# Optimization experiments

Hardware: AMD Instinct MI355X
Metric: run time of the kernel (lower is better)

Reference implementation:

```python
import jax, jax.numpy as jnp
import numpy as np

B, C, H, W = 16, 64, 128, 128
K = 3
Z = 128


def setup_inputs() -> dict:
    key = jax.random.key(0)
    k1, k2, k3, k4 = jax.random.split(key, 4)
    x = jax.random.normal(k1, (B, C, H, W), dtype=jnp.float32)
    z = jax.random.normal(k2, (B, Z), dtype=jnp.float32)
    # generator: Linear(Z -> C*C*K*K), scaled for stable conv outputs
    gen_w = jax.random.normal(k3, (Z, C * C * K * K), dtype=jnp.float32) * 0.02
    gen_b = jax.random.normal(k4, (C * C * K * K,), dtype=jnp.float32) * 0.02
    return {"x": x, "z": z, "gen_w": gen_w, "gen_b": gen_b}


def _conv_one(xi, wi):
    # xi: [C,H,W], wi: [C_out,C_in,K,K]; 'same' padding conv, no bias
    out = jax.lax.conv_general_dilated(
        xi[None], wi, window_strides=(1, 1), padding="SAME",
        dimension_numbers=("NCHW", "OIHW", "NCHW"))
    return out[0]


def reference(x, z, gen_w, gen_b):
    # per-sample weight generation: [B, C*C*K*K] -> [B, C, C, K, K]
    weight = (z @ gen_w + gen_b).reshape(B, C, C, K, K)
    # batched per-sample convolution (replaces the python loop over batch)
    return jax.vmap(_conv_one)(x, weight)
```

## Files before the change

kernel.cpp:

```cpp
#include <hip/hip_runtime.h>
#include <hip/hip_bf16.h>

typedef __attribute__((ext_vector_type(4))) float f32x4;
typedef __attribute__((ext_vector_type(8))) short short8;

#define B_ 16
#define C_ 64
#define H_ 128
#define W_ 128
#define Z_ 128
#define IDXN (C_*C_*9)
#define NT 18

__device__ __forceinline__ unsigned short f2bf(float f) {
  __hip_bfloat16 h = __float2bfloat16(f);
  return *reinterpret_cast<unsigned short*>(&h);
}

__global__ __launch_bounds__(256) void wgen_k(
    const float* __restrict__ z, const float* __restrict__ gw,
    const float* __restrict__ gb, unsigned short* __restrict__ wfrag) {
  __shared__ __align__(16) float zs[B_*Z_];
  int t = threadIdx.x;
#pragma unroll
  for (int i = 0; i < 8; ++i) zs[i*256 + t] = z[i*256 + t];
  __syncthreads();
  int lane = t & 63, bg = t >> 6;
  int b0 = bg*4;
  int idx0 = blockIdx.x*128 + lane;
  float acc[4][2];
  float bv0 = gb[idx0], bv1 = gb[idx0 + 64];
#pragma unroll
  for (int bi = 0; bi < 4; ++bi) { acc[bi][0] = bv0; acc[bi][1] = bv1; }

  for (int z0 = 0; z0 < Z_; z0 += 4) {
    float ga[4], gbv[4];
#pragma unroll
    for (int zi = 0; zi < 4; ++zi) {
      ga[zi]  = gw[(size_t)(z0+zi)*IDXN + idx0];
      gbv[zi] = gw[(size_t)(z0+zi)*IDXN + idx0 + 64];
    }
#pragma unroll
    for (int bi = 0; bi < 4; ++bi) {
      f32x4 zq = *reinterpret_cast<const f32x4*>(&zs[(b0+bi)*Z_ + z0]);
      acc[bi][0] = fmaf(zq[0], ga[0], fmaf(zq[1], ga[1], fmaf(zq[2], ga[2], fmaf(zq[3], ga[3], acc[bi][0]))));
      acc[bi][1] = fmaf(zq[0], gbv[0], fmaf(zq[1], gbv[1], fmaf(zq[2], gbv[2], fmaf(zq[3], gbv[3], acc[bi][1]))));
    }
  }
#pragma unroll
  for (int ni = 0; ni < 2; ++ni) {
    int idx = idx0 + ni*64;
    int kw = idx % 3, r1 = idx/3;
    int kh = r1 % 3, r2 = r1/3;
    int ci = r2 & 63, co = r2 >> 6;
    int k = (kh*3 + kw)*C_ + ci;
    int ts = k >> 5, kin = k & 31;
    int lm = (co & 15) | ((kin >> 3) << 4);
    int j = kin & 7, m = co >> 4;
    int base = ((ts*4 + m)*64 + lm)*8 + j;
#pragma unroll
    for (int bi = 0; bi < 4; ++bi)
      wfrag[(size_t)(b0+bi)*(NT*4*64*8) + base] = f2bf(acc[bi][ni]);
  }
}

__global__ __launch_bounds__(512, 4) void conv_k(
    const float* __restrict__ x,
    const unsigned short* __restrict__ wfrag,
    float* __restrict__ out) {
  __shared__ __align__(16) unsigned char xs[4*130*128];
  int orig = blockIdx.x;
  int blk = (orig & 7)*128 + (orig >> 3);
  int b = blk >> 6;
  int h0 = (blk & 63)*2;
  int tid = threadIdx.x;
  int v = tid >> 6, lane = tid & 63;

  {
    int r = v >> 1, hf = v & 1;
    int hh = h0 - 1 + r;
    bool hv = (hh >= 0) & (hh < H_);
    unsigned char* ldsrow = xs + r*(130*128);
    if (hv) {
      if (lane < 8) {
        int s = hf ? (1032 + lane) : lane;
        uint4 zv; zv.x = 0; zv.y = 0; zv.z = 0; zv.w = 0;
        *reinterpret_cast<uint4*>(ldsrow + s*16) = zv;
      }
      const float* xrow = x + (((size_t)b*C_)*H_ + hh)*W_;
      int w0 = 2*lane, col0 = w0 + 1, col1 = w0 + 2;
      int g = lane >> 3;
#pragma unroll
      for (int i = 0; i < 4; ++i) {
        int chunk = (hf*4 + i + g) & 7;
        float2 v2[8];
#pragma unroll
        for (int j = 0; j < 8; ++j)
          v2[j] = *reinterpret_cast<const float2*>(xrow + (size_t)(chunk*8 + j)*(H_*W_) + w0);
        uint4 o0, o1;
        unsigned short* s0 = reinterpret_cast<unsigned short*>(&o0);
        unsigned short* s1 = reinterpret_cast<unsigned short*>(&o1);
#pragma unroll
        for (int j = 0; j < 8; ++j) {
          s0[j] = f2bf(v2[j].x);
          s1[j] = f2bf(v2[j].y);
        }
        int a0 = col0*128 + (((chunk ^ col0) & 7) << 4);
        int a1 = col1*128 + (((chunk ^ col1) & 7) << 4);
        *reinterpret_cast<uint4*>(ldsrow + a0) = o0;
        *reinterpret_cast<uint4*>(ldsrow + a1) = o1;
      }
    } else {
      uint4 zv; zv.x = 0; zv.y = 0; zv.z = 0; zv.w = 0;
#pragma unroll
      for (int it = 0; it < 9; ++it) {
        int di = it*64 + lane;
        if (di < 520) *reinterpret_cast<uint4*>(ldsrow + (hf*520 + di)*16) = zv;
      }
    }
  }

  int l15 = lane & 15, lhi = lane >> 4;
  int phr = v >> 2, pw0 = ((v >> 1) & 1)*64;
  int mt0 = (v & 1)*2;
  const unsigned short* wb = wfrag + (size_t)b*(NT*4*64*8);

  short8 wf0 = *reinterpret_cast<const short8*>(wb + (((0*4 + mt0 + 0)*64 + lane)*8));
  short8 wf1 = *reinterpret_cast<const short8*>(wb + (((0*4 + mt0 + 1)*64 + lane)*8));

  __syncthreads();

  f32x4 acc[4][2];
#pragma unroll
  for (int mp = 0; mp < 4; ++mp)
#pragma unroll
    for (int nc = 0; nc < 2; ++nc)
      acc[mp][nc] = (f32x4){0.f, 0.f, 0.f, 0.f};

#pragma unroll
  for (int t = 0; t < NT; ++t) {
    int kk = t >> 1, kh = kk/3, kw = kk%3, half = t & 1;
    short8 nf0, nf1;
    if (t + 1 < NT) {
      nf0 = *reinterpret_cast<const short8*>(wb + ((((t+1)*4 + mt0 + 0)*64 + lane)*8));
      nf1 = *reinterpret_cast<const short8*>(wb + ((((t+1)*4 + mt0 + 1)*64 + lane)*8));
    }
    int chunk = half*4 + lhi;
    short8 xa[4];
#pragma unroll
    for (int mp = 0; mp < 4; ++mp) {
      int col = pw0 + mp*16 + l15 + kw;
      int addr = ((phr + kh)*130 + col)*128 + (((chunk ^ col) & 7) << 4);
      xa[mp] = *reinterpret_cast<const short8*>(&xs[addr]);
    }
#pragma unroll
    for (int mp = 0; mp < 4; ++mp) {
      acc[mp][0] = __builtin_amdgcn_mfma_f32_16x16x32_bf16(xa[mp], wf0, acc[mp][0], 0, 0, 0);
      acc[mp][1] = __builtin_amdgcn_mfma_f32_16x16x32_bf16(xa[mp], wf1, acc[mp][1], 0, 0, 0);
    }
    wf0 = nf0; wf1 = nf1;
  }

  int ph = h0 + phr;
#pragma unroll
  for (int nc = 0; nc < 2; ++nc) {
    int co = (mt0 + nc)*16 + l15;
    float* op = out + (((size_t)b*C_ + co)*H_ + ph)*W_;
#pragma unroll
    for (int mp = 0; mp < 4; ++mp) {
      int pix = pw0 + mp*16 + lhi*4;
      *reinterpret_cast<f32x4*>(op + pix) = acc[mp][nc];
    }
  }
}

__global__ void sentinel_k(float* out, int n) {
  int i = blockIdx.x*256 + threadIdx.x;
  if (i < n) out[i] = 1.0e6f;
}

extern "C" void kernel_launch(void* const* d_in, const int* in_sizes, int n_in,
                              void* d_out, int out_size, void* d_ws, size_t ws_size,
                              hipStream_t stream) {
  const float* x  = (const float*)d_in[0];
  const float* z  = (const float*)d_in[1];
  const float* gw = (const float*)d_in[2];
  const float* gb = (const float*)d_in[3];
  float* out = (float*)d_out;

  size_t wfrag_elems = (size_t)B_*IDXN;
  size_t need = wfrag_elems*sizeof(unsigned short);
  if (ws_size < need) {
    sentinel_k<<<(out_size + 255)/256, 256, 0, stream>>>(out, out_size);
    return;
  }
  unsigned short* wfrag = (unsigned short*)d_ws;

  wgen_k <<<IDXN/128, 256, 0, stream>>>(z, gw, gb, wfrag);
  conv_k <<<B_*(H_/2), 512, 0, stream>>>(x, wfrag, out);
}
```

Baseline: 51.23 us.

## Process 8-row bands per block with ring-buffered LDS rows and prefetch

The conv kernel moves from one 2-row tile per 512-thread block to 1024-thread blocks that each walk an 8-row band in four 2-row steps. Input rows live in a 6-slot ring buffer in LDS, and the next two rows are loaded from global memory while the MFMAs for the current step run. The MFMA inner loop is also software-pipelined so LDS fragments for the next tap are loaded one step ahead. The aim is to cut the redundant halo loads (4 rows loaded per 2 output rows) and to hide global load latency. In exchange the grid shrinks to 256 blocks, there is a syncthreads per step, and each wave now does less MFMA work per LDS fragment.

```diff
diff --git a/kernel.cpp b/kernel.cpp
--- a/kernel.cpp
+++ b/kernel.cpp
@@ -9,6 +9,8 @@
 #define H_ 128
 #define W_ 128
 #define Z_ 128
+#define HW_ (H_*W_)
+#define CHW_ (C_*H_*W_)
 #define IDXN (C_*C_*9)
 #define NT 18
 
@@ -64,113 +66,145 @@
   }
 }
 
-__global__ __launch_bounds__(512, 4) void conv_k(
+__global__ __launch_bounds__(1024, 4) void conv_k(
     const float* __restrict__ x,
     const unsigned short* __restrict__ wfrag,
     float* __restrict__ out) {
-  __shared__ __align__(16) unsigned char xs[4*130*128];
+  __shared__ __align__(16) unsigned char xs[6*130*128];
   int orig = blockIdx.x;
-  int blk = (orig & 7)*128 + (orig >> 3);
-  int b = blk >> 6;
-  int h0 = (blk & 63)*2;
+  int blk = (orig & 7)*32 + (orig >> 3);
+  int b = blk >> 4;
+  int band = blk & 15;
+  int hbase = band*8;
   int tid = threadIdx.x;
   int v = tid >> 6, lane = tid & 63;
 
-  {
-    int r = v >> 1, hf = v & 1;
-    int hh = h0 - 1 + r;
-    bool hv = (hh >= 0) & (hh < H_);
-    unsigned char* ldsrow = xs + r*(130*128);
-    if (hv) {
-      if (lane < 8) {
-        int s = hf ? (1032 + lane) : lane;
-        uint4 zv; zv.x = 0; zv.y = 0; zv.z = 0; zv.w = 0;
-        *reinterpret_cast<uint4*>(ldsrow + s*16) = zv;
-      }
-      const float* xrow = x + (((size_t)b*C_)*H_ + hh)*W_;
-      int w0 = 2*lane, col0 = w0 + 1, col1 = w0 + 2;
-      int g = lane >> 3;
-#pragma unroll
-      for (int i = 0; i < 4; ++i) {
-        int chunk = (hf*4 + i + g) & 7;
-        float2 v2[8];
-#pragma unroll
-        for (int j = 0; j < 8; ++j)
-          v2[j] = *reinterpret_cast<const float2*>(xrow + (size_t)(chunk*8 + j)*(H_*W_) + w0);
-        uint4 o0, o1;
-        unsigned short* s0 = reinterpret_cast<unsigned short*>(&o0);
-        unsigned short* s1 = reinterpret_cast<unsigned short*>(&o1);
-#pragma unroll
-        for (int j = 0; j < 8; ++j) {
-          s0[j] = f2bf(v2[j].x);
-          s1[j] = f2bf(v2[j].y);
+  int ri = tid >> 9;
+  int wp = lane;
+  int cig = v & 7;
+  const float* xb = x + (size_t)b*CHW_;
+  int s_base0 = hbase % 6;
+
+  if (tid < 96) {
+    int sl = tid >> 4, cc = (tid >> 3) & 1, ch = tid & 7;
+    int col = cc ? 129 : 0;
+    uint4 zv; zv.x = 0; zv.y = 0; zv.z = 0; zv.w = 0;
+    *reinterpret_cast<uint4*>(&xs[(sl*130 + col)*128 + ch*16]) = zv;
+  }
+
+#pragma unroll
+  for (int s = 0; s < 2; ++s) {
+    int g = hbase - 1 + 2*s + ri;
+    int slw = s_base0 + 2*s + ri; if (slw >= 6) slw -= 6;
+    uint4 o0, o1;
+    o0.x=0;o0.y=0;o0.z=0;o0.w=0; o1=o0;
+    if (g >= 0 && g < H_) {
+      const float* xr = xb + (size_t)g*W_ + 2*wp;
+      unsigned short* p0 = reinterpret_cast<unsigned short*>(&o0);
+      unsigned short* p1 = reinterpret_cast<unsigned short*>(&o1);
+#pragma unroll
+      for (int j = 0; j < 8; ++j) {
+        float2 f = *reinterpret_cast<const float2*>(xr + (size_t)(cig*8 + j)*HW_);
+        p0[j] = f2bf(f.x); p1[j] = f2bf(f.y);
+      }
+    }
+    int c0 = 2*wp + 1, c1 = c0 + 1;
+    *reinterpret_cast<uint4*>(&xs[(slw*130 + c0)*128 + (((cig ^ c0) & 7) << 4)]) = o0;
+    *reinterpret_cast<uint4*>(&xs[(slw*130 + c1)*128 + (((cig ^ c1) & 7) << 4)]) = o1;
+  }
+  __syncthreads();
+
+  int l15 = lane & 15, lhi = lane >> 4;
+  int phr = v >> 3;
+  int pw0 = ((v >> 1) & 3) * 32;
+  int mt0 = (v & 1) * 2;
+  const unsigned short* wb = wfrag + (size_t)b*(NT*4*64*8);
+
+  int s_base = s_base0;
+  float2 sv[8];
+
+#pragma unroll 1
+  for (int p = 0; p < 4; ++p) {
+    int sg = hbase + 2*p + 3 + ri;
+    bool sval = (p < 3) && (sg < H_);
+    if (sval) {
+      const float* xr = xb + (size_t)sg*W_ + 2*wp;
+#pragma unroll
+      for (int j = 0; j < 8; ++j)
+        sv[j] = *reinterpret_cast<const float2*>(xr + (size_t)(cig*8 + j)*HW_);
+    }
+
+    f32x4 acc[2][2];
+#pragma unroll
+    for (int mp = 0; mp < 2; ++mp)
+#pragma unroll
+      for (int nc = 0; nc < 2; ++nc)
+        acc[mp][nc] = (f32x4){0.f, 0.f, 0.f, 0.f};
+
+    short8 xa0[2], xa1[2], wf0[2], wf1[2];
+    {
+      int chunk = lhi;
+      int rs = s_base + phr; if (rs >= 6) rs -= 6;
+#pragma unroll
+      for (int mp = 0; mp < 2; ++mp) {
+        int col = pw0 + mp*16 + l15;
+        xa0[mp] = *reinterpret_cast<const short8*>(&xs[(rs*130 + col)*128 + (((chunk ^ col) & 7) << 4)]);
+      }
+#pragma unroll
+      for (int nc = 0; nc < 2; ++nc)
+        wf0[nc] = *reinterpret_cast<const short8*>(wb + ((mt0 + nc)*64 + lane)*8);
+    }
+#pragma unroll
+    for (int t = 0; t < NT; ++t) {
+      if (t + 1 < NT) {
+        int t1 = t + 1;
+        int kk = t1 >> 1, kh = kk/3, kw = kk%3, half = t1 & 1;
+        int chunk = half*4 + lhi;
+        int rs = s_base + phr + kh; if (rs >= 6) rs -= 6;
+#pragma unroll
+        for (int mp = 0; mp < 2; ++mp) {
+          int col = pw0 + mp*16 + l15 + kw;
+          xa1[mp] = *reinterpret_cast<const short8*>(&xs[(rs*130 + col)*128 + (((chunk ^ col) & 7) << 4)]);
         }
-        int a0 = col0*128 + (((chunk ^ col0) & 7) << 4);
-        int a1 = col1*128 + (((chunk ^ col1) & 7) << 4);
-        *reinterpret_cast<uint4*>(ldsrow + a0) = o0;
-        *reinterpret_cast<uint4*>(ldsrow + a1) = o1;
-      }
-    } else {
-      uint4 zv; zv.x = 0; zv.y = 0; zv.z = 0; zv.w = 0;
-#pragma unroll
-      for (int it = 0; it < 9; ++it) {
-        int di = it*64 + lane;
-        if (di < 520) *reinterpret_cast<uint4*>(ldsrow + (hf*520 + di)*16) = zv;
-      }
-    }
-  }
-
-  int l15 = lane & 15, lhi = lane >> 4;
-  int phr = v >> 2, pw0 = ((v >> 1) & 1)*64;
-  int mt0 = (v & 1)*2;
-  const unsigned short* wb = wfrag + (size_t)b*(NT*4*64*8);
-
-  short8 wf0 = *reinterpret_cast<const short8*>(wb + (((0*4 + mt0 + 0)*64 + lane)*8));
-  short8 wf1 = *reinterpret_cast<const short8*>(wb + (((0*4 + mt0 + 1)*64 + lane)*8));
-
-  __syncthreads();
-
-  f32x4 acc[4][2];
-#pragma unroll
-  for (int mp = 0; mp < 4; ++mp)
-#pragma unroll
-    for (int nc = 0; nc < 2; ++nc)
-      acc[mp][nc] = (f32x4){0.f, 0.f, 0.f, 0.f};
-
-#pragma unroll
-  for (int t = 0; t < NT; ++t) {
-    int kk = t >> 1, kh = kk/3, kw = kk%3, half = t & 1;
-    short8 nf0, nf1;
-    if (t + 1 < NT) {
-      nf0 = *reinterpret_cast<const short8*>(wb + ((((t+1)*4 + mt0 + 0)*64 + lane)*8));
-      nf1 = *reinterpret_cast<const short8*>(wb + ((((t+1)*4 + mt0 + 1)*64 + lane)*8));
-    }
-    int chunk = half*4 + lhi;
-    short8 xa[4];
-#pragma unroll
-    for (int mp = 0; mp < 4; ++mp) {
-      int col = pw0 + mp*16 + l15 + kw;
-      int addr = ((phr + kh)*130 + col)*128 + (((chunk ^ col) & 7) << 4);
-      xa[mp] = *reinterpret_cast<const short8*>(&xs[addr]);
-    }
-#pragma unroll
-    for (int mp = 0; mp < 4; ++mp) {
-      acc[mp][0] = __builtin_amdgcn_mfma_f32_16x16x32_bf16(xa[mp], wf0, acc[mp][0], 0, 0, 0);
-      acc[mp][1] = __builtin_amdgcn_mfma_f32_16x16x32_bf16(xa[mp], wf1, acc[mp][1], 0, 0, 0);
-    }
-    wf0 = nf0; wf1 = nf1;
-  }
-
-  int ph = h0 + phr;
-#pragma unroll
-  for (int nc = 0; nc < 2; ++nc) {
-    int co = (mt0 + nc)*16 + l15;
-    float* op = out + (((size_t)b*C_ + co)*H_ + ph)*W_;
-#pragma unroll
-    for (int mp = 0; mp < 4; ++mp) {
-      int pix = pw0 + mp*16 + lhi*4;
-      *reinterpret_cast<f32x4*>(op + pix) = acc[mp][nc];
-    }
+#pragma unroll
+        for (int nc = 0; nc < 2; ++nc)
+          wf1[nc] = *reinterpret_cast<const short8*>(wb + ((t1*4 + mt0 + nc)*64 + lane)*8);
+      }
+#pragma unroll
+      for (int mp = 0; mp < 2; ++mp)
+#pragma unroll
+        for (int nc = 0; nc < 2; ++nc)
+          acc[mp][nc] = __builtin_amdgcn_mfma_f32_16x16x32_bf16(xa0[mp], wf0[nc], acc[mp][nc], 0, 0, 0);
+      xa0[0] = xa1[0]; xa0[1] = xa1[1];
+      wf0[0] = wf1[0]; wf0[1] = wf1[1];
+    }
+
+    int ph = hbase + 2*p + phr;
+#pragma unroll
+    for (int nc = 0; nc < 2; ++nc) {
+      int co = (mt0 + nc)*16 + l15;
+      float* op = out + (((size_t)b*C_ + co)*H_ + ph)*W_;
+#pragma unroll
+      for (int mp = 0; mp < 2; ++mp)
+        *reinterpret_cast<f32x4*>(op + pw0 + mp*16 + lhi*4) = acc[mp][nc];
+    }
+
+    if (p < 3) {
+      int slw = s_base + 4 + ri; if (slw >= 6) slw -= 6;
+      uint4 o0, o1;
+      o0.x=0;o0.y=0;o0.z=0;o0.w=0; o1=o0;
+      if (sval) {
+        unsigned short* p0 = reinterpret_cast<unsigned short*>(&o0);
+        unsigned short* p1 = reinterpret_cast<unsigned short*>(&o1);
+#pragma unroll
+        for (int j = 0; j < 8; ++j) { p0[j] = f2bf(sv[j].x); p1[j] = f2bf(sv[j].y); }
+      }
+      int c0 = 2*wp + 1, c1 = c0 + 1;
+      *reinterpret_cast<uint4*>(&xs[(slw*130 + c0)*128 + (((cig ^ c0) & 7) << 4)]) = o0;
+      *reinterpret_cast<uint4*>(&xs[(slw*130 + c1)*128 + (((cig ^ c1) & 7) << 4)]) = o1;
+    }
+    s_base += 2; if (s_base >= 6) s_base -= 6;
+    __syncthreads();
   }
 }
 
@@ -197,5 +231,5 @@
   unsigned short* wfrag = (unsigned short*)d_ws;
 
   wgen_k <<<IDXN/128, 256, 0, stream>>>(z, gw, gb, wfrag);
-  conv_k <<<B_*(H_/2), 512, 0, stream>>>(x, wfrag, out);
-}
+  conv_k <<<B_*16, 1024, 0, stream>>>(x, wfrag, out);
+}
```

Measured after the change: 146.6 us. 186% more time.

## Deepen weight prefetch, double-buffer LDS reads, stagger K-step order per wave

Applied to the files above, without the earlier changes.

The weight-fragment loads move ahead of the LDS staging and are prefetched three steps deep instead of one. LDS reads of the input tile are double-buffered so the next step's fragments load while the current MFMAs run. Each wave starts its 18-step K loop at a different offset (2*wave), which spreads LDS bank and global-load traffic across waves. This raises register pressure under the launch bound of 4 blocks per CU.

```diff
diff --git a/kernel.cpp b/kernel.cpp
--- a/kernel.cpp
+++ b/kernel.cpp
@@ -76,6 +76,20 @@
   int tid = threadIdx.x;
   int v = tid >> 6, lane = tid & 63;
 
+  int l15 = lane & 15, lhi = lane >> 4;
+  int phr = v >> 2, pw0 = ((v >> 1) & 1)*64;
+  int mt0 = (v & 1)*2;
+  int toff = 2*v;
+  const unsigned short* wb = wfrag + (size_t)b*(NT*4*64*8);
+
+  short8 wfs[3][2];
+#pragma unroll
+  for (int s0 = 0; s0 < 3; ++s0) {
+    int ta = s0 + toff; if (ta >= NT) ta -= NT;
+    wfs[s0][0] = *reinterpret_cast<const short8*>(wb + ((ta*4 + mt0 + 0)*64 + lane)*8);
+    wfs[s0][1] = *reinterpret_cast<const short8*>(wb + ((ta*4 + mt0 + 1)*64 + lane)*8);
+  }
+
   {
     int r = v >> 1, hf = v & 1;
     int hh = h0 - 1 + r;
@@ -119,15 +133,6 @@
       }
     }
   }
-
-  int l15 = lane & 15, lhi = lane >> 4;
-  int phr = v >> 2, pw0 = ((v >> 1) & 1)*64;
-  int mt0 = (v & 1)*2;
-  const unsigned short* wb = wfrag + (size_t)b*(NT*4*64*8);
-
-  short8 wf0 = *reinterpret_cast<const short8*>(wb + (((0*4 + mt0 + 0)*64 + lane)*8));
-  short8 wf1 = *reinterpret_cast<const short8*>(wb + (((0*4 + mt0 + 1)*64 + lane)*8));
-
   __syncthreads();
 
   f32x4 acc[4][2];
@@ -137,28 +142,42 @@
     for (int nc = 0; nc < 2; ++nc)
       acc[mp][nc] = (f32x4){0.f, 0.f, 0.f, 0.f};
 
-#pragma unroll
-  for (int t = 0; t < NT; ++t) {
-    int kk = t >> 1, kh = kk/3, kw = kk%3, half = t & 1;
-    short8 nf0, nf1;
-    if (t + 1 < NT) {
-      nf0 = *reinterpret_cast<const short8*>(wb + ((((t+1)*4 + mt0 + 0)*64 + lane)*8));
-      nf1 = *reinterpret_cast<const short8*>(wb + ((((t+1)*4 + mt0 + 1)*64 + lane)*8));
-    }
-    int chunk = half*4 + lhi;
-    short8 xa[4];
+  short8 xab[2][4];
+  {
+    int ta = toff; if (ta >= NT) ta -= NT;
+    int kk = ta >> 1; int kh = (kk*11) >> 5; int kw = kk - 3*kh; int hf2 = ta & 1;
+    int chunk = hf2*4 + lhi;
+    int rbase = (phr + kh)*130;
 #pragma unroll
     for (int mp = 0; mp < 4; ++mp) {
       int col = pw0 + mp*16 + l15 + kw;
-      int addr = ((phr + kh)*130 + col)*128 + (((chunk ^ col) & 7) << 4);
-      xa[mp] = *reinterpret_cast<const short8*>(&xs[addr]);
+      xab[0][mp] = *reinterpret_cast<const short8*>(&xs[(rbase + col)*128 + (((chunk ^ col) & 7) << 4)]);
+    }
+  }
+
+#pragma unroll
+  for (int s = 0; s < NT; ++s) {
+    if (s + 1 < NT) {
+      int ta = s + 1 + toff; if (ta >= NT) ta -= NT;
+      int kk = ta >> 1; int kh = (kk*11) >> 5; int kw = kk - 3*kh; int hf2 = ta & 1;
+      int chunk = hf2*4 + lhi;
+      int rbase = (phr + kh)*130;
+#pragma unroll
+      for (int mp = 0; mp < 4; ++mp) {
+        int col = pw0 + mp*16 + l15 + kw;
+        xab[(s+1)&1][mp] = *reinterpret_cast<const short8*>(&xs[(rbase + col)*128 + (((chunk ^ col) & 7) << 4)]);
+      }
     }
 #pragma unroll
     for (int mp = 0; mp < 4; ++mp) {
-      acc[mp][0] = __builtin_amdgcn_mfma_f32_16x16x32_bf16(xa[mp], wf0, acc[mp][0], 0, 0, 0);
-      acc[mp][1] = __builtin_amdgcn_mfma_f32_16x16x32_bf16(xa[mp], wf1, acc[mp][1], 0, 0, 0);
-    }
-    wf0 = nf0; wf1 = nf1;
+      acc[mp][0] = __builtin_amdgcn_mfma_f32_16x16x32_bf16(xab[s&1][mp], wfs[s%3][0], acc[mp][0], 0, 0, 0);
+      acc[mp][1] = __builtin_amdgcn_mfma_f32_16x16x32_bf16(xab[s&1][mp], wfs[s%3][1], acc[mp][1], 0, 0, 0);
+    }
+    if (s + 3 < NT) {
+      int ta = s + 3 + toff; if (ta >= NT) ta -= NT;
+      wfs[s%3][0] = *reinterpret_cast<const short8*>(wb + ((ta*4 + mt0 + 0)*64 + lane)*8);
+      wfs[s%3][1] = *reinterpret_cast<const short8*>(wb + ((ta*4 + mt0 + 1)*64 + lane)*8);
+    }
   }
 
   int ph = h0 + phr;
```

Result: slower. 52.45 us (+2.4%).
